# Kernel optimization log

Hardware: AMD Instinct MI355X
Metric: run time of the kernel (lower is better)

Reference implementation:

```python
import jax, jax.numpy as jnp
import numpy as np


def setup_inputs() -> dict:
    key = jax.random.key(0)
    ks = jax.random.split(key, 8)
    B, C, H, W = 8, 256, 64, 64
    r = 32  # channels // reduction
    return {
        "x": jax.random.normal(ks[0], (B, C, H, W), dtype=jnp.float32),
        "wq": jax.random.normal(ks[1], (r, C), dtype=jnp.float32) * 0.02,
        "bq": jax.random.normal(ks[2], (r,), dtype=jnp.float32) * 0.02,
        "wk": jax.random.normal(ks[3], (r, C), dtype=jnp.float32) * 0.02,
        "bk": jax.random.normal(ks[4], (r,), dtype=jnp.float32) * 0.02,
        "wv": jax.random.normal(ks[5], (C, C), dtype=jnp.float32) * 0.02,
        "bv": jax.random.normal(ks[6], (C,), dtype=jnp.float32) * 0.02,
        "gamma": jax.random.normal(ks[7], (1,), dtype=jnp.float32),
    }


def reference(x, wq, bq, wk, bk, wv, bv, gamma):
    B, C, H, W = x.shape
    N = H * W
    r = wq.shape[0]
    scale = r ** (-0.5)
    xf = x.reshape(B, C, N)  # flatten spatial tokens
    # 1x1 convs == per-pixel linear projections
    q = jnp.einsum("rc,bcn->bnr", wq, xf) + bq  # (B, N, r)
    k = jnp.einsum("rc,bcn->brn", wk, xf) + bk[:, None]  # (B, r, N)
    v = jnp.einsum("dc,bcn->bdn", wv, xf) + bv[:, None]  # (B, C, N)
    attn = jax.nn.softmax(jnp.einsum("bnr,brm->bnm", q, k) * scale, axis=-1)  # (B, N, N)
    # out[b,c,n] = sum_m v[b,c,m] * attn[b,n,m]
    out = jnp.einsum("bdm,bnm->bdn", v, attn).reshape(B, C, H, W)
    return x + gamma[0] * out
```

## Files before the change

kernel.cpp:

```cpp
#include <hip/hip_runtime.h>
#include <hip/hip_bf16.h>


typedef float  f32x4   __attribute__((ext_vector_type(4)));
typedef short  short8  __attribute__((ext_vector_type(8)));
typedef unsigned short ushort4v __attribute__((ext_vector_type(4)));
typedef unsigned short ushort8v __attribute__((ext_vector_type(8)));

__device__ __forceinline__ unsigned short f2bf(float f) {
    __hip_bfloat16 h = __float2bfloat16(f);
    return __builtin_bit_cast(unsigned short, h);
}

__global__ __launch_bounds__(256) void wconv_kernel(
    const float* __restrict__ wq, const float* __restrict__ wk,
    const float* __restrict__ wv, unsigned short* __restrict__ Wall)
{
    int i4 = blockIdx.x * 256 + threadIdx.x;
    int e = i4 * 4;
    const float* src; int off;
    if (e < 8192)       { src = wq; off = e; }
    else if (e < 16384) { src = wk; off = e - 8192; }
    else                { src = wv; off = e - 16384; }
    f32x4 v = *(const f32x4*)(src + off);
    ushort4v u;
#pragma unroll
    for (int j = 0; j < 4; ++j) u[j] = f2bf(v[j]);
    *(ushort4v*)(Wall + e) = u;
}

__global__ __launch_bounds__(256) void xpose_kernel(
    const float* __restrict__ x, unsigned short* __restrict__ xT, int C, int N)
{
    const int t  = threadIdx.x;
    const int n  = blockIdx.x * 256 + t;
    const int c0 = blockIdx.y * 64;
    const int b  = blockIdx.z;
    const float* xb = x + ((size_t)b * C + c0) * N + n;

    unsigned short tmp[64];
#pragma unroll
    for (int i = 0; i < 64; ++i)
        tmp[i] = f2bf(xb[(size_t)i * N]);

    unsigned short* dst = xT + ((size_t)b * N + n) * 256 + c0;
#pragma unroll
    for (int i = 0; i < 8; ++i) {
        ushort8v u;
#pragma unroll
        for (int j = 0; j < 8; ++j) u[j] = tmp[i * 8 + j];
        *(ushort8v*)(dst + i * 8) = u;
    }
}

__global__ __launch_bounds__(256) void projmm_kernel(
    const unsigned short* __restrict__ xT,
    const unsigned short* __restrict__ Wall,
    const float* __restrict__ bq, const float* __restrict__ bk,
    const float* __restrict__ bv,
    unsigned short* __restrict__ qa,
    unsigned short* __restrict__ ka,
    unsigned char* __restrict__ vt8,
    int N, float scale)
{
    __shared__ __align__(16) unsigned short xs[64 * 136];
    __shared__ __align__(16) unsigned short ws[64 * 136];

    const int t  = threadIdx.x;
    const int l  = t & 63;
    const int w  = t >> 6;
    const int qi = l & 15;
    const int g  = l >> 4;
    const int n0 = blockIdx.x * 64;
    const int o0 = blockIdx.y * 64;
    const int b  = blockIdx.z;
    const int tile = n0 >> 6;
    const unsigned short* xTb = xT + (size_t)b * N * 256;

    const f32x4 zero4 = {0.f, 0.f, 0.f, 0.f};
    f32x4 acc[4];
#pragma unroll
    for (int nf = 0; nf < 4; ++nf) acc[nf] = zero4;

    for (int kp = 0; kp < 2; ++kp) {
        if (kp) __syncthreads();
        for (int it = w; it < 34; it += 4) {
            int isw = it >= 17;
            int it2 = isw ? it - 17 : it;
            unsigned short* lbase = (isw ? ws : xs) + it2 * 512;
            int ch  = it2 * 64 + l;
            int row = ch / 17;
            int c16 = ch - row * 17;
            int cc  = c16 > 15 ? 15 : c16;
            const unsigned short* src = isw
                ? (Wall + (size_t)(o0 + row) * 256 + kp * 128 + cc * 8)
                : (xTb + (size_t)(n0 + row) * 256 + kp * 128 + cc * 8);
            __builtin_amdgcn_global_load_lds(
                (const __attribute__((address_space(1))) unsigned int*)src,
                (__attribute__((address_space(3))) unsigned int*)lbase, 16, 0, 0);
        }
        __syncthreads();

#pragma unroll
        for (int ks = 0; ks < 4; ++ks) {
            short8 af;
            {
                const unsigned short* ap = ws + (w * 16 + qi) * 136 + ks * 32 + g * 4;
                ushort4v lo = *(const ushort4v*)ap;
                ushort4v hi = *(const ushort4v*)(ap + 16);
#pragma unroll
                for (int j = 0; j < 4; ++j) { af[j] = (short)lo[j]; af[4 + j] = (short)hi[j]; }
            }
#pragma unroll
            for (int nf = 0; nf < 4; ++nf) {
                short8 bf;
                const unsigned short* bp = xs + (nf * 16 + qi) * 136 + ks * 32 + g * 4;
                ushort4v lo = *(const ushort4v*)bp;
                ushort4v hi = *(const ushort4v*)(bp + 16);
#pragma unroll
                for (int j = 0; j < 4; ++j) { bf[j] = (short)lo[j]; bf[4 + j] = (short)hi[j]; }
                acc[nf] = __builtin_amdgcn_mfma_f32_16x16x32_bf16(af, bf, acc[nf], 0, 0, 0);
            }
        }
    }

    if (o0 == 0) {
        const float* bias = (w < 2) ? bq : bk;
        float sc = (w < 2) ? scale : 1.0f;
        unsigned short* dst = (w < 2) ? qa : ka;
#pragma unroll
        for (int nf = 0; nf < 4; ++nf) {
            ushort4v u;
#pragma unroll
            for (int j = 0; j < 4; ++j) {
                int r = (w & 1) * 16 + g * 4 + j;
                u[j] = f2bf((acc[nf][j] + bias[r]) * sc);
            }
            *(ushort4v*)(dst + ((((size_t)b * 64 + tile) * 4 + nf) * 64 + g * 16 + qi) * 8 + (w & 1) * 4) = u;
        }
    } else {
        unsigned char* vtb = vt8 + ((size_t)b * 64 + tile) * 16384;
#pragma unroll
        for (int nf = 0; nf < 4; ++nf) {
            int m = nf * 16 + qi;
            int G   = ((m & 32) ? 4 : 0) + ((m >> 2) & 3);
            int pos = ((m >> 4) & 1) * 4 + (m & 3);
#pragma unroll
            for (int j = 0; j < 4; ++j) {
                int c = o0 - 64 + w * 16 + g * 4 + j;
                int r = __builtin_amdgcn_cvt_pk_fp8_f32(acc[nf][j] + bv[c], 0.f, 0, false);
                vtb[(size_t)c * 64 + ((G ^ ((c >> 1) & 7)) << 3) + pos] = (unsigned char)(r & 0xFF);
            }
        }
    }
}

__global__ __launch_bounds__(512, 4) void attn_kernel(
    const float* __restrict__ x,
    const unsigned short* __restrict__ qa,
    const unsigned short* __restrict__ ka,
    const unsigned char* __restrict__ vt8,
    const float* __restrict__ gamma,
    float* __restrict__ out, int C, int N)
{
    __shared__ __align__(16) unsigned char vs[4][16384];
    __shared__ float mlb[4][64];

    const int t  = threadIdx.x;
    const int l  = t & 63;
    const int w  = t >> 6;
    const int qi = l & 15;
    const int g  = l >> 4;
    const int qg = w & 3;
    const int kh = w >> 2;
    const int tile_q = blockIdx.x;
    const int b  = blockIdx.y;

    const f32x4 zero4 = {0.f, 0.f, 0.f, 0.f};

    short8 qfrag = *(const short8*)(
        qa + ((((size_t)b * 64 + tile_q) * 4 + qg) * 64 + l) * 8);

    const unsigned short* kab = ka + ((size_t)b * 64) * 2048 + (size_t)kh * 1024 + (size_t)l * 8;
    const unsigned char*  vtb = vt8 + ((size_t)b * 64) * 16384;

    auto stage = [&](int buf, int tl) {
        const unsigned char* src = vtb + (size_t)tl * 16384 + w * 2048 + l * 16;
        unsigned char* dst = &vs[buf][w * 2048 + l * 16];
#pragma unroll
        for (int i = 0; i < 2; ++i)
            __builtin_amdgcn_global_load_lds(
                (const __attribute__((address_space(1))) unsigned int*)(src + i * 1024),
                (__attribute__((address_space(3))) unsigned int*)(dst + i * 1024), 16, 0, 0);
    };

    f32x4 o_[16];
#pragma unroll
    for (int cf = 0; cf < 16; ++cf) o_[cf] = zero4;
    float lsum = 0.f;
    long acur;

    auto packP = [&](const f32x4& s0, const f32x4& s1) -> long {
        float p[8];
#pragma unroll
        for (int j = 0; j < 4; ++j) { p[j] = __expf(s0[j]); p[4 + j] = __expf(s1[j]); }
#pragma unroll
        for (int j = 0; j < 8; ++j) lsum += p[j];
        int w0 = __builtin_amdgcn_cvt_pk_fp8_f32(p[0], p[1], 0, false);
        w0 = __builtin_amdgcn_cvt_pk_fp8_f32(p[2], p[3], w0, true);
        int w1 = __builtin_amdgcn_cvt_pk_fp8_f32(p[4], p[5], 0, false);
        w1 = __builtin_amdgcn_cvt_pk_fp8_f32(p[6], p[7], w1, true);
        return (long)(((unsigned long long)(unsigned int)w0) |
                      ((unsigned long long)(unsigned int)w1 << 32));
    };

    const int voff = (((kh << 2) | g) ^ ((qi >> 1) & 7)) << 3;
    auto pv = [&](int buf) {
        const unsigned char* vrow = &vs[buf][qi * 64 + voff];
#pragma unroll
        for (int cf = 0; cf < 16; ++cf) {
            long v8 = *(const long*)(vrow + cf * 1024);
            o_[cf] = __builtin_amdgcn_mfma_f32_16x16x32_fp8_fp8(acur, v8, o_[cf], 0, 0, 0);
        }
    };

    stage(0, 0);
    stage(1, 1);
    short8 kcur0 = *(const short8*)(kab);
    short8 kcur1 = *(const short8*)(kab + 512);
    {
        f32x4 s0 = __builtin_amdgcn_mfma_f32_16x16x32_bf16(kcur0, qfrag, zero4, 0, 0, 0);
        f32x4 s1 = __builtin_amdgcn_mfma_f32_16x16x32_bf16(kcur1, qfrag, zero4, 0, 0, 0);
        acur = packP(s0, s1);
    }
    {
        const unsigned short* kn = kab + 2048;
        kcur0 = *(const short8*)(kn);
        kcur1 = *(const short8*)(kn + 512);
    }
    __syncthreads();

    for (int p = 0; p < 32; ++p) {
        const int t0 = 2 * p;
        if (p < 31) {
            stage((t0 + 2) & 3, t0 + 2);
            stage((t0 + 3) & 3, t0 + 3);
        }

        f32x4 s0 = __builtin_amdgcn_mfma_f32_16x16x32_bf16(kcur0, qfrag, zero4, 0, 0, 0);
        f32x4 s1 = __builtin_amdgcn_mfma_f32_16x16x32_bf16(kcur1, qfrag, zero4, 0, 0, 0);
        if (p < 31) {
            const unsigned short* kn = kab + (size_t)(t0 + 2) * 2048;
            kcur0 = *(const short8*)(kn);
            kcur1 = *(const short8*)(kn + 512);
        }
        pv(t0 & 3);
        acur = packP(s0, s1);

        f32x4 r0, r1;
        if (p < 31) {
            r0 = __builtin_amdgcn_mfma_f32_16x16x32_bf16(kcur0, qfrag, zero4, 0, 0, 0);
            r1 = __builtin_amdgcn_mfma_f32_16x16x32_bf16(kcur1, qfrag, zero4, 0, 0, 0);
            const unsigned short* kn = kab + (size_t)(t0 + 3) * 2048;
            kcur0 = *(const short8*)(kn);
            kcur1 = *(const short8*)(kn + 512);
        }
        pv((t0 + 1) & 3);
        if (p < 31)
            acur = packP(r0, r1);

        __syncthreads();
    }

    float l_run = lsum;
    l_run += __shfl_xor(l_run, 16);
    l_run += __shfl_xor(l_run, 32);

    float* cbuf = (float*)vs;
    const int lx = l & 31;
    float* bp = cbuf + ((qg * 64) + l) * 32;
    if (kh == 1) {
        mlb[qg][l] = l_run;
#pragma unroll
        for (int cf = 0; cf < 8; ++cf)
#pragma unroll
            for (int j = 0; j < 4; ++j) bp[(cf * 4 + j) ^ lx] = o_[cf][j];
    }
    __syncthreads();

    float cj[4];
    const float gm = gamma[0];
    const float* xb = x + (size_t)b * C * N;
    float* ob = out + (size_t)b * C * N;
    const int ncol = tile_q * 64 + qg * 16 + g * 4;

    if (kh == 0) {
        float lt = l_run + mlb[qg][l];
        float c0 = gm / lt;
#pragma unroll
        for (int j = 0; j < 4; ++j) cj[j] = __shfl(c0, g * 4 + j);
#pragma unroll
        for (int cf = 0; cf < 8; ++cf) {
            int c = cf * 16 + qi;
            f32x4 xv = *(const f32x4*)(xb + (size_t)c * N + ncol);
            f32x4 ov;
#pragma unroll
            for (int j = 0; j < 4; ++j)
                ov[j] = xv[j] + (o_[cf][j] + bp[(cf * 4 + j) ^ lx]) * cj[j];
            *(f32x4*)(ob + (size_t)c * N + ncol) = ov;
        }
    }
    __syncthreads();

    if (kh == 1) {
#pragma unroll
        for (int cf = 0; cf < 8; ++cf)
#pragma unroll
            for (int j = 0; j < 4; ++j) bp[(cf * 4 + j) ^ lx] = o_[8 + cf][j];
    }
    __syncthreads();

    if (kh == 0) {
#pragma unroll
        for (int cf = 0; cf < 8; ++cf) {
            int c = (8 + cf) * 16 + qi;
            f32x4 xv = *(const f32x4*)(xb + (size_t)c * N + ncol);
            f32x4 ov;
#pragma unroll
            for (int j = 0; j < 4; ++j)
                ov[j] = xv[j] + (o_[8 + cf][j] + bp[(cf * 4 + j) ^ lx]) * cj[j];
            *(f32x4*)(ob + (size_t)c * N + ncol) = ov;
        }
    }
}

extern "C" void kernel_launch(void* const* d_in, const int* in_sizes, int n_in,
                              void* d_out, int out_size, void* d_ws, size_t ws_size,
                              hipStream_t stream) {
    const float* x     = (const float*)d_in[0];
    const float* wq    = (const float*)d_in[1];
    const float* bq    = (const float*)d_in[2];
    const float* wk    = (const float*)d_in[3];
    const float* bk    = (const float*)d_in[4];
    const float* wv    = (const float*)d_in[5];
    const float* bv    = (const float*)d_in[6];
    const float* gamma = (const float*)d_in[7];
    float* out = (float*)d_out;

    const int B = 8, C = 256, N = 4096;
    const float scale = 0.17677669529663687f;

    unsigned short* qa   = (unsigned short*)d_ws;
    unsigned short* ka   = qa + (size_t)B * 64 * 4 * 64 * 8;
    unsigned short* xT   = ka + (size_t)B * 64 * 4 * 64 * 8;
    unsigned short* Wall = xT + (size_t)B * N * 256;
    unsigned char*  vt8  = (unsigned char*)(Wall + 81920);

    wconv_kernel<<<80, 256, 0, stream>>>(wq, wk, wv, Wall);
    xpose_kernel<<<dim3(N / 256, C / 64, B), 256, 0, stream>>>(x, xT, C, N);
    projmm_kernel<<<dim3(N / 64, 5, B), 256, 0, stream>>>(
        xT, Wall, bq, bk, bv, qa, ka, vt8, N, scale);
    attn_kernel<<<dim3(N / 64, B), 512, 0, stream>>>(x, qa, ka, vt8, gamma, out, C, N);
}
```

Baseline: 113.6 us.

## Stage K tiles through LDS and restructure attention loop to one tile per barrier

K fragments are now loaded asynchronously into LDS alongside the V tiles via global_load_lds, instead of being read with direct global register loads. The main loop processes one key tile per iteration, using a manual vmcnt wait plus barrier in place of __syncthreads, with a 2-tile-ahead prefetch into a 4-deep ring buffer. The softmax-sum exchange buffer moves into the enlarged shared buffer. This is meant to hide K load latency and simplify the software pipeline, at the cost of more LDS per block (which may reduce occupancy) and twice as many barriers.

Result: faster. 109.7 us (-3.4%).

```diff
diff --git a/kernel.cpp b/kernel.cpp
--- a/kernel.cpp
+++ b/kernel.cpp
@@ -163,8 +163,7 @@
     const float* __restrict__ gamma,
     float* __restrict__ out, int C, int N)
 {
-    __shared__ __align__(16) unsigned char vs[4][16384];
-    __shared__ float mlb[4][64];
+    __shared__ __align__(16) unsigned char vs[4][20480];
 
     const int t  = threadIdx.x;
     const int l  = t & 63;
@@ -181,24 +180,33 @@
     short8 qfrag = *(const short8*)(
         qa + ((((size_t)b * 64 + tile_q) * 4 + qg) * 64 + l) * 8);
 
-    const unsigned short* kab = ka + ((size_t)b * 64) * 2048 + (size_t)kh * 1024 + (size_t)l * 8;
-    const unsigned char*  vtb = vt8 + ((size_t)b * 64) * 16384;
+    const unsigned char* kab_b = (const unsigned char*)(ka + ((size_t)b * 64) * 2048);
+    const unsigned char* vtb   = vt8 + ((size_t)b * 64) * 16384;
 
     auto stage = [&](int buf, int tl) {
-        const unsigned char* src = vtb + (size_t)tl * 16384 + w * 2048 + l * 16;
-        unsigned char* dst = &vs[buf][w * 2048 + l * 16];
-#pragma unroll
-        for (int i = 0; i < 2; ++i)
-            __builtin_amdgcn_global_load_lds(
-                (const __attribute__((address_space(1))) unsigned int*)(src + i * 1024),
-                (__attribute__((address_space(3))) unsigned int*)(dst + i * 1024), 16, 0, 0);
+        const unsigned char* vsrc = vtb + (size_t)tl * 16384 + w * 2048 + l * 16;
+        unsigned char* vdst = &vs[buf][w * 2048 + l * 16];
+        __builtin_amdgcn_global_load_lds(
+            (const __attribute__((address_space(1))) unsigned int*)vsrc,
+            (__attribute__((address_space(3))) unsigned int*)vdst, 16, 0, 0);
+        __builtin_amdgcn_global_load_lds(
+            (const __attribute__((address_space(1))) unsigned int*)(vsrc + 1024),
+            (__attribute__((address_space(3))) unsigned int*)(vdst + 1024), 16, 0, 0);
+        const unsigned char* ksrc = kab_b + (size_t)tl * 4096 + w * 512 + l * 4;
+        unsigned char* kdst = &vs[buf][16384 + w * 512 + l * 4];
+        __builtin_amdgcn_global_load_lds(
+            (const __attribute__((address_space(1))) unsigned int*)ksrc,
+            (__attribute__((address_space(3))) unsigned int*)kdst, 4, 0, 0);
+        __builtin_amdgcn_global_load_lds(
+            (const __attribute__((address_space(1))) unsigned int*)(ksrc + 256),
+            (__attribute__((address_space(3))) unsigned int*)(kdst + 256), 4, 0, 0);
     };
 
     f32x4 o_[16];
 #pragma unroll
     for (int cf = 0; cf < 16; ++cf) o_[cf] = zero4;
     float lsum = 0.f;
-    long acur;
+    long acur = 0;
 
     auto packP = [&](const f32x4& s0, const f32x4& s1) -> long {
         float p[8];
@@ -226,61 +234,36 @@
 
     stage(0, 0);
     stage(1, 1);
-    short8 kcur0 = *(const short8*)(kab);
-    short8 kcur1 = *(const short8*)(kab + 512);
-    {
-        f32x4 s0 = __builtin_amdgcn_mfma_f32_16x16x32_bf16(kcur0, qfrag, zero4, 0, 0, 0);
-        f32x4 s1 = __builtin_amdgcn_mfma_f32_16x16x32_bf16(kcur1, qfrag, zero4, 0, 0, 0);
+
+    for (int tl = 0; tl < 64; ++tl) {
+        asm volatile("s_waitcnt vmcnt(4)\n\ts_barrier" ::: "memory");
+        __builtin_amdgcn_sched_barrier(0);
+
+        if (tl < 62) stage((tl + 2) & 3, tl + 2);
+
+        const unsigned char* kb2 = &vs[tl & 3][16384 + kh * 2048 + l * 16];
+        short8 kf0 = *(const short8*)kb2;
+        short8 kf1 = *(const short8*)(kb2 + 1024);
+        f32x4 s0 = __builtin_amdgcn_mfma_f32_16x16x32_bf16(kf0, qfrag, zero4, 0, 0, 0);
+        f32x4 s1 = __builtin_amdgcn_mfma_f32_16x16x32_bf16(kf1, qfrag, zero4, 0, 0, 0);
+
+        if (tl) pv((tl - 1) & 3);
+
         acur = packP(s0, s1);
     }
-    {
-        const unsigned short* kn = kab + 2048;
-        kcur0 = *(const short8*)(kn);
-        kcur1 = *(const short8*)(kn + 512);
-    }
-    __syncthreads();
-
-    for (int p = 0; p < 32; ++p) {
-        const int t0 = 2 * p;
-        if (p < 31) {
-            stage((t0 + 2) & 3, t0 + 2);
-            stage((t0 + 3) & 3, t0 + 3);
-        }
-
-        f32x4 s0 = __builtin_amdgcn_mfma_f32_16x16x32_bf16(kcur0, qfrag, zero4, 0, 0, 0);
-        f32x4 s1 = __builtin_amdgcn_mfma_f32_16x16x32_bf16(kcur1, qfrag, zero4, 0, 0, 0);
-        if (p < 31) {
-            const unsigned short* kn = kab + (size_t)(t0 + 2) * 2048;
-            kcur0 = *(const short8*)(kn);
-            kcur1 = *(const short8*)(kn + 512);
-        }
-        pv(t0 & 3);
-        acur = packP(s0, s1);
-
-        f32x4 r0, r1;
-        if (p < 31) {
-            r0 = __builtin_amdgcn_mfma_f32_16x16x32_bf16(kcur0, qfrag, zero4, 0, 0, 0);
-            r1 = __builtin_amdgcn_mfma_f32_16x16x32_bf16(kcur1, qfrag, zero4, 0, 0, 0);
-            const unsigned short* kn = kab + (size_t)(t0 + 3) * 2048;
-            kcur0 = *(const short8*)(kn);
-            kcur1 = *(const short8*)(kn + 512);
-        }
-        pv((t0 + 1) & 3);
-        if (p < 31)
-            acur = packP(r0, r1);
-
-        __syncthreads();
-    }
+    pv(3);
 
     float l_run = lsum;
     l_run += __shfl_xor(l_run, 16);
     l_run += __shfl_xor(l_run, 32);
 
+    __syncthreads();
     float* cbuf = (float*)vs;
+    float* lex  = cbuf + 8192;
     const int lx = l & 31;
     float* bp = cbuf + ((qg * 64) + l) * 32;
     if (kh == 1) {
-        mlb[qg][l] = l_run;
+        lex[qg * 64 + l] = l_run;
 #pragma unroll
         for (int cf = 0; cf < 8; ++cf)
 #pragma unroll
@@ -295,7 +278,7 @@
     const int ncol = tile_q * 64 + qg * 16 + g * 4;
 
     if (kh == 0) {
-        float lt = l_run + mlb[qg][l];
+        float lt = l_run + lex[qg * 64 + l];
         float c0 = gm / lt;
 #pragma unroll
         for (int j = 0; j < 4; ++j) cj[j] = __shfl(c0, g * 4 + j);
```
